# Performance work log

Measured on AMD Instinct MI355X. Metric: run time of the kernel, lower is better.

Reference implementation:

```python
import jax, jax.numpy as jnp
import numpy as np

N, D, R, E = 10000, 1024, 8, 80000


def setup_inputs() -> dict:
    key = jax.random.key(0)
    ks = jax.random.split(key, 8)
    s = 1.0 / np.sqrt(D)
    x = jax.random.normal(ks[0], (N, D), dtype=jnp.float32)
    edge_index = jax.random.randint(ks[1], (2, E), 0, N, dtype=jnp.int64)
    edge_type = jax.random.randint(ks[2], (E,), 0, R, dtype=jnp.int64)
    weight = jax.random.normal(ks[3], (R, D, D), dtype=jnp.float32) * s  # per-relation W_r
    root = jax.random.normal(ks[4], (D, D), dtype=jnp.float32) * s      # root/self-loop weight
    bias = jnp.zeros((D,), dtype=jnp.float32)
    w_gate = jax.random.normal(ks[5], (2 * D, D), dtype=jnp.float32) * (1.0 / np.sqrt(2 * D))
    b_gate = jnp.zeros((D,), dtype=jnp.float32)
    return {"x": x, "edge_index": edge_index, "edge_type": edge_type,
            "weight": weight, "root": root, "bias": bias,
            "w_gate": w_gate, "b_gate": b_gate}


def _rgcn(x, edge_index, edge_type, weight, root, bias):
    # PyG RGCNConv (aggr='mean'): per relation r, mean-aggregate x[src] into dst,
    # then transform by W_r (aggregate-then-transform, equivalent by linearity).
    src, dst = edge_index[0], edge_index[1]
    msgs = x[src]                                   # [E, D] gather
    out = x @ root + bias                           # root/self connection
    n = x.shape[0]
    for r in range(weight.shape[0]):                # small fixed relation loop
        mask = (edge_type == r).astype(x.dtype)     # [E]
        sums = jax.ops.segment_sum(msgs * mask[:, None], dst, num_segments=n)
        cnt = jax.ops.segment_sum(mask, dst, num_segments=n)
        mean = sums / jnp.maximum(cnt, 1.0)[:, None]
        out = out + mean @ weight[r]
    return out


def reference(x, edge_index, edge_type, weight, root, bias, w_gate, b_gate):
    u = _rgcn(x, edge_index, edge_type, weight, root, bias)
    # dropout p=0 -> identity
    z = jnp.concatenate([u, x], axis=1) @ w_gate + b_gate
    h = jnp.tanh(u) * z + x * (1.0 - z)
    return h
```

## Files before the change

kernel.cpp:

```cpp
#include <hip/hip_runtime.h>
#include <math.h>

typedef unsigned short u16;
typedef __attribute__((ext_vector_type(8))) short bf16x8;
typedef __attribute__((ext_vector_type(4))) float f32x4;

static constexpr int kN = 10000;
static constexpr int kNpad = 10240;
static constexpr int kD = 1024;
static constexpr int kR = 8;
static constexpr int kE = 80000;
static constexpr int kKz = 2 * kD;
static constexpr int kCrows = kNpad * (kR + 1);

#define GLB(p) ((const __attribute__((address_space(1))) unsigned int*)(const void*)(p))
#define LDSP(p) ((__attribute__((address_space(3))) unsigned int*)(p))

__device__ __forceinline__ u16 f2bf(float f) {
    union { float f; unsigned int i; } c; c.f = f;
    unsigned int u = c.i;
    return (u16)((u + 0x7FFFu + ((u >> 16) & 1u)) >> 16);
}
__device__ __forceinline__ float bf2f(u16 u) {
    union { unsigned int i; float f; } c; c.i = ((unsigned int)u) << 16;
    return c.f;
}
__device__ __forceinline__ ushort4 f2bf4(float4 v) {
    ushort4 o; o.x = f2bf(v.x); o.y = f2bf(v.y); o.z = f2bf(v.z); o.w = f2bf(v.w);
    return o;
}

__global__ void zero16(uint4* __restrict__ p, long n16) {
    long i = (long)blockIdx.x * blockDim.x + threadIdx.x;
    long st = (long)gridDim.x * blockDim.x;
    uint4 z = make_uint4(0, 0, 0, 0);
    for (; i < n16; i += st) p[i] = z;
}

__global__ void mark_edges(const int* __restrict__ src, const int* __restrict__ dst,
                           const int* __restrict__ etype,
                           int* __restrict__ cntd, int* __restrict__ flag) {
    int e = blockIdx.x * blockDim.x + threadIdx.x;
    if (e < kE) {
        atomicAdd(&cntd[dst[e]], 1);
        flag[etype[e] * kN + src[e]] = 1;
    }
}

__global__ __launch_bounds__(1024) void scan_combo(const int* __restrict__ cnt,
                                                   int* __restrict__ rowptr,
                                                   int* __restrict__ cursor,
                                                   const int* __restrict__ flag,
                                                   int* __restrict__ row_src,
                                                   int* __restrict__ pos_tab,
                                                   int* __restrict__ relcnt9) {
    __shared__ int wsum[16];
    __shared__ int carry;
    const int tid = threadIdx.x;
    const int lane = tid & 63;
    const int w = tid >> 6;

    if (blockIdx.x == 0) {
        if (tid == 0) carry = 0;
        const int nchunk = (kN + 1024) / 1024;
        for (int ch = 0; ch < nchunk; ++ch) {
            int idx = ch * 1024 + tid;
            int v = (idx < kN) ? cnt[idx] : 0;
            int s = v;
#pragma unroll
            for (int off = 1; off < 64; off <<= 1) {
                int t = __shfl_up(s, off, 64);
                if (lane >= off) s += t;
            }
            if (lane == 63) wsum[w] = s;
            __syncthreads();
            if (w == 0 && lane < 16) {
                int t = wsum[lane];
#pragma unroll
                for (int off = 1; off < 16; off <<= 1) {
                    int tt = __shfl_up(t, off, 64);
                    if (lane >= off) t += tt;
                }
                wsum[lane] = t;
            }
            __syncthreads();
            int wpre = (w > 0) ? wsum[w - 1] : 0;
            int incl = s + wpre + carry;
            int excl = incl - v;
            if (idx <= kN) rowptr[idx] = excl;
            if (idx < kN) cursor[idx] = 0;
            __syncthreads();
            if (tid == 1023) carry = incl;
            __syncthreads();
        }
        return;
    }

    const int rr = blockIdx.x - 1;
    if (rr == kR) {
        for (int i = tid; i < kNpad; i += 1024) row_src[i] = i;
        if (tid == 0) relcnt9[0] = kN;
        return;
    }
    const int r = rr;
    const int base = kNpad * (r + 1);
    if (tid == 0) carry = 0;
    const int nchunk = (kN + 1023) / 1024;
    for (int ch = 0; ch < nchunk; ++ch) {
        int idx = ch * 1024 + tid;
        int v = (idx < kN) ? flag[r * kN + idx] : 0;
        int s = v;
#pragma unroll
        for (int off = 1; off < 64; off <<= 1) {
            int t = __shfl_up(s, off, 64);
            if (lane >= off) s += t;
        }
        if (lane == 63) wsum[w] = s;
        __syncthreads();
        if (w == 0 && lane < 16) {
            int t = wsum[lane];
#pragma unroll
            for (int off = 1; off < 16; off <<= 1) {
                int tt = __shfl_up(t, off, 64);
                if (lane >= off) t += tt;
            }
            wsum[lane] = t;
        }
        __syncthreads();
        int wpre = (w > 0) ? wsum[w - 1] : 0;
        int incl = s + wpre + carry;
        int excl = incl - v;
        if (idx < kN && v) {
            row_src[base + excl] = idx;
            pos_tab[r * kN + idx] = base + excl;
        }
        __syncthreads();
        if (tid == 1023) carry = incl;
        __syncthreads();
    }
    if (tid == 0) relcnt9[r + 1] = carry;
}

__global__ void fill_edges(const int* __restrict__ src, const int* __restrict__ dst,
                           const int* __restrict__ etype, const int* __restrict__ rowptr,
                           int* __restrict__ cursor, const int* __restrict__ pos_tab,
                           int* __restrict__ erec) {
    int e = blockIdx.x * blockDim.x + threadIdx.x;
    if (e < kE) {
        int d = dst[e], r = etype[e], s = src[e];
        int pos = rowptr[d] + atomicAdd(&cursor[d], 1);
        erec[pos] = (pos_tab[r * kN + s] << 3) | r;
    }
}

__global__ void prep_ga(const float* __restrict__ x, u16* __restrict__ ga) {
    int row = blockIdx.x;
    int c = threadIdx.x << 2;
    if (row < kN) {
        float4 v = *reinterpret_cast<const float4*>(x + (size_t)row * kD + c);
        *reinterpret_cast<ushort4*>(ga + (size_t)row * kKz + kD + c) = f2bf4(v);
    } else {
        ushort4 z4;
        z4.x = 0; z4.y = 0; z4.z = 0; z4.w = 0;
        *reinterpret_cast<ushort4*>(ga + (size_t)row * kKz + c) = z4;
        *reinterpret_cast<ushort4*>(ga + (size_t)row * kKz + kD + c) = z4;
    }
}

__global__ void transpose_all(const float* __restrict__ root,
                              const float* __restrict__ weight,
                              const float* __restrict__ wgate,
                              u16* __restrict__ Bt9, u16* __restrict__ wg_t) {
    const int z = blockIdx.z;
    const float* S;
    u16* D;
    int ldD;
    if (z == 0)       { S = root;                              D = Bt9;                       ldD = kD; }
    else if (z <= 8)  { S = weight + (size_t)(z - 1) * kD * kD; D = Bt9 + (size_t)z * kD * kD; ldD = kD; }
    else              { S = wgate + (size_t)(z - 9) * kD * kD;  D = wg_t + (size_t)(z - 9) * kD; ldD = kKz; }
    __shared__ float t[32][33];
    int c0 = blockIdx.x * 32, r0 = blockIdx.y * 32;
    int x = threadIdx.x, y = threadIdx.y;
#pragma unroll
    for (int i = 0; i < 32; i += 8)
        t[y + i][x] = S[(size_t)(r0 + y + i) * kD + c0 + x];
    __syncthreads();
#pragma unroll
    for (int i = 0; i < 32; i += 8)
        D[(size_t)(c0 + y + i) * ldD + r0 + x] = f2bf(t[x][y + i]);
}

__global__ __launch_bounds__(256) void aggregate(const u16* __restrict__ yc,
                                                 const float* __restrict__ bias,
                                                 const int* __restrict__ rowptr,
                                                 const int* __restrict__ erec,
                                                 u16* __restrict__ ga) {
    const int d = blockIdx.x;
    const int c = threadIdx.x << 2;
    const int e0 = rowptr[d], e1 = rowptr[d + 1];

    __shared__ int cc8[kR];
    __shared__ float rs[kR];
    if (threadIdx.x < kR) cc8[threadIdx.x] = 0;
    __syncthreads();
    if (threadIdx.x < 64) {
        for (int e = e0 + threadIdx.x; e < e1; e += 64)
            atomicAdd(&cc8[erec[e] & 7], 1);
    }
    __syncthreads();
    if (threadIdx.x < kR)
        rs[threadIdx.x] = 1.0f / fmaxf((float)cc8[threadIdx.x], 1.0f);
    __syncthreads();

    ushort4 rv = *reinterpret_cast<const ushort4*>(yc + (size_t)d * kD + c);
    float4 bv = *reinterpret_cast<const float4*>(bias + c);
    float4 acc = make_float4(bf2f(rv.x) + bv.x, bf2f(rv.y) + bv.y,
                             bf2f(rv.z) + bv.z, bf2f(rv.w) + bv.w);

    int e = e0;
    for (; e + 3 < e1; e += 4) {
        int rec0 = erec[e], rec1 = erec[e + 1], rec2 = erec[e + 2], rec3 = erec[e + 3];
        ushort4 v0 = *reinterpret_cast<const ushort4*>(yc + (size_t)(rec0 >> 3) * kD + c);
        ushort4 v1 = *reinterpret_cast<const ushort4*>(yc + (size_t)(rec1 >> 3) * kD + c);
        ushort4 v2 = *reinterpret_cast<const ushort4*>(yc + (size_t)(rec2 >> 3) * kD + c);
        ushort4 v3 = *reinterpret_cast<const ushort4*>(yc + (size_t)(rec3 >> 3) * kD + c);
        float s0 = rs[rec0 & 7], s1 = rs[rec1 & 7], s2 = rs[rec2 & 7], s3 = rs[rec3 & 7];
        acc.x += s0 * bf2f(v0.x); acc.y += s0 * bf2f(v0.y);
        acc.z += s0 * bf2f(v0.z); acc.w += s0 * bf2f(v0.w);
        acc.x += s1 * bf2f(v1.x); acc.y += s1 * bf2f(v1.y);
        acc.z += s1 * bf2f(v1.z); acc.w += s1 * bf2f(v1.w);
        acc.x += s2 * bf2f(v2.x); acc.y += s2 * bf2f(v2.y);
        acc.z += s2 * bf2f(v2.z); acc.w += s2 * bf2f(v2.w);
        acc.x += s3 * bf2f(v3.x); acc.y += s3 * bf2f(v3.y);
        acc.z += s3 * bf2f(v3.z); acc.w += s3 * bf2f(v3.w);
    }
    for (; e < e1; ++e) {
        int rec = erec[e];
        float sc = rs[rec & 7];
        ushort4 v = *reinterpret_cast<const ushort4*>(yc + (size_t)(rec >> 3) * kD + c);
        acc.x += sc * bf2f(v.x); acc.y += sc * bf2f(v.y);
        acc.z += sc * bf2f(v.z); acc.w += sc * bf2f(v.w);
    }
    *reinterpret_cast<ushort4*>(ga + (size_t)d * kKz + c) = f2bf4(acc);
}

__global__ __launch_bounds__(512, 2) void gemm_compact(
    const u16* __restrict__ xb, int ldx,
    const u16* __restrict__ Bt9,
    const int* __restrict__ row_src, const int* __restrict__ relcnt9,
    u16* __restrict__ yc)
{
    const int t0 = blockIdx.y;
    const int relidx = t0 / 40;
    const int lt = t0 - relidx * 40;
    if (lt * 256 >= relcnt9[relidx]) return;

    __shared__ u16 sA[2][256 * 64];
    __shared__ u16 sB[2][256 * 64];

    const int tid = threadIdx.x;
    const int wave = tid >> 6;
    const int lane = tid & 63;

    const int row0 = t0 * 256;
    const int col0 = blockIdx.x * 256;

    const int s_row = tid >> 3;
    const int s_src = ((tid & 7) ^ (s_row & 7)) * 8;
    const int wbase = wave * 512;

    const u16* gA[4];
    const u16* gB[4];
#pragma unroll
    for (int q = 0; q < 4; ++q) {
        gA[q] = xb + (size_t)row_src[row0 + q * 64 + s_row] * ldx + s_src;
        gB[q] = Bt9 + (size_t)(relidx * kD + col0 + q * 64 + s_row) * kD + s_src;
    }

    auto stageA = [&](int b, int h) {
        u16* dA = &sA[b][0];
#pragma unroll
        for (int q = 2 * h; q < 2 * h + 2; ++q) {
            __builtin_amdgcn_global_load_lds(GLB(gA[q]), LDSP(dA + q * 4096 + wbase), 16, 0, 0);
            gA[q] += 64;
        }
    };
    auto stageB = [&](int b, int h) {
        u16* dB = &sB[b][0];
#pragma unroll
        for (int q = 2 * h; q < 2 * h + 2; ++q) {
            __builtin_amdgcn_global_load_lds(GLB(gB[q]), LDSP(dB + q * 4096 + wbase), 16, 0, 0);
            gB[q] += 64;
        }
    };

    const int wm = (wave >> 2) * 128;
    const int wn = (wave & 3) * 64;
    const int fm = lane & 15;
    const int g4 = lane >> 4;
    const int pc0 = ((g4) ^ (fm & 7)) * 8;
    const int pc1 = ((4 | g4) ^ (fm & 7)) * 8;

    f32x4 zf = {0.0f, 0.0f, 0.0f, 0.0f};
    f32x4 acc[8][4];
#pragma unroll
    for (int i = 0; i < 8; ++i)
#pragma unroll
        for (int j = 0; j < 4; ++j) acc[i][j] = zf;

    constexpr int T = kD / 64;
    stageA(0, 0); stageA(0, 1); stageB(0, 0); stageB(0, 1);
    stageB(1, 0); stageB(1, 1);

    bf16x8 af[8], bfl[4], bfh[4];

    for (int t = 0; t < T; ++t) {
        const int cb = t & 1, nb = cb ^ 1;
        const bool pf1 = (t + 1 < T);
        const bool pf2 = (t + 2 < T);
        const u16* cA = sA[cb];
        const u16* cB = sB[cb];

        if (pf1) stageA(nb, 0);
        if (t < T - 1) asm volatile("s_waitcnt vmcnt(6)" ::: "memory");
        else           asm volatile("s_waitcnt vmcnt(0)" ::: "memory");
        __builtin_amdgcn_s_barrier();
        asm volatile("" ::: "memory");
#pragma unroll
        for (int i = 0; i < 4; ++i) {
            af[2 * i]     = *reinterpret_cast<const bf16x8*>(&cA[(wm + i * 16 + fm) * 64 + pc0]);
            af[2 * i + 1] = *reinterpret_cast<const bf16x8*>(&cA[(wm + i * 16 + fm) * 64 + pc1]);
        }
#pragma unroll
        for (int j = 0; j < 2; ++j) {
            bfl[2 * j]     = *reinterpret_cast<const bf16x8*>(&cB[(wn + j * 16 + fm) * 64 + pc0]);
            bfl[2 * j + 1] = *reinterpret_cast<const bf16x8*>(&cB[(wn + j * 16 + fm) * 64 + pc1]);
        }
        __builtin_amdgcn_s_setprio(1);
#pragma unroll
        for (int i = 0; i < 4; ++i)
#pragma unroll
            for (int j = 0; j < 2; ++j) {
                acc[i][j] = __builtin_amdgcn_mfma_f32_16x16x32_bf16(bfl[2 * j], af[2 * i], acc[i][j], 0, 0, 0);
                acc[i][j] = __builtin_amdgcn_mfma_f32_16x16x32_bf16(bfl[2 * j + 1], af[2 * i + 1], acc[i][j], 0, 0, 0);
            }
        __builtin_amdgcn_s_setprio(0);

#pragma unroll
        for (int j = 0; j < 2; ++j) {
            bfh[2 * j]     = *reinterpret_cast<const bf16x8*>(&cB[(wn + 32 + j * 16 + fm) * 64 + pc0]);
            bfh[2 * j + 1] = *reinterpret_cast<const bf16x8*>(&cB[(wn + 32 + j * 16 + fm) * 64 + pc1]);
        }
        if (pf1) stageA(nb, 1);
        asm volatile("" ::: "memory");
        __builtin_amdgcn_s_barrier();
        asm volatile("" ::: "memory");
        __builtin_amdgcn_s_setprio(1);
#pragma unroll
        for (int i = 0; i < 4; ++i)
#pragma unroll
            for (int j = 0; j < 2; ++j) {
                acc[i][2 + j] = __builtin_amdgcn_mfma_f32_16x16x32_bf16(bfh[2 * j], af[2 * i], acc[i][2 + j], 0, 0, 0);
                acc[i][2 + j] = __builtin_amdgcn_mfma_f32_16x16x32_bf16(bfh[2 * j + 1], af[2 * i + 1], acc[i][2 + j], 0, 0, 0);
            }
        __builtin_amdgcn_s_setprio(0);

#pragma unroll
        for (int i = 0; i < 4; ++i) {
            af[2 * i]     = *reinterpret_cast<const bf16x8*>(&cA[(wm + 64 + i * 16 + fm) * 64 + pc0]);
            af[2 * i + 1] = *reinterpret_cast<const bf16x8*>(&cA[(wm + 64 + i * 16 + fm) * 64 + pc1]);
        }
        asm volatile("" ::: "memory");
        __builtin_amdgcn_s_barrier();
        asm volatile("" ::: "memory");
        __builtin_amdgcn_s_setprio(1);
#pragma unroll
        for (int i = 0; i < 4; ++i)
#pragma unroll
            for (int j = 0; j < 2; ++j) {
                acc[4 + i][2 + j] = __builtin_amdgcn_mfma_f32_16x16x32_bf16(bfh[2 * j], af[2 * i], acc[4 + i][2 + j], 0, 0, 0);
                acc[4 + i][2 + j] = __builtin_amdgcn_mfma_f32_16x16x32_bf16(bfh[2 * j + 1], af[2 * i + 1], acc[4 + i][2 + j], 0, 0, 0);
            }
        __builtin_amdgcn_s_setprio(0);

        if (pf2) { stageB(cb, 0); stageB(cb, 1); }
        asm volatile("" ::: "memory");
        __builtin_amdgcn_s_barrier();
        asm volatile("" ::: "memory");
        __builtin_amdgcn_s_setprio(1);
#pragma unroll
        for (int i = 0; i < 4; ++i)
#pragma unroll
            for (int j = 0; j < 2; ++j) {
                acc[4 + i][j] = __builtin_amdgcn_mfma_f32_16x16x32_bf16(bfl[2 * j], af[2 * i], acc[4 + i][j], 0, 0, 0);
                acc[4 + i][j] = __builtin_amdgcn_mfma_f32_16x16x32_bf16(bfl[2 * j + 1], af[2 * i + 1], acc[4 + i][j], 0, 0, 0);
            }
        __builtin_amdgcn_s_setprio(0);
    }

    const int cq = g4 * 4;
#pragma unroll
    for (int i = 0; i < 8; ++i) {
        int row = row0 + wm + i * 16 + fm;
#pragma unroll
        for (int j = 0; j < 4; ++j) {
            int col = col0 + wn + j * 16 + cq;
            f32x4 v = acc[i][j];
            ushort4 o;
            o.x = f2bf(v[0]); o.y = f2bf(v[1]); o.z = f2bf(v[2]); o.w = f2bf(v[3]);
            *reinterpret_cast<ushort4*>(yc + (size_t)row * kD + col) = o;
        }
    }
}

__global__ __launch_bounds__(256, 3) void gemm_mfma_gate(
    const u16* __restrict__ A, int lda,
    const u16* __restrict__ Bt, int ldb, int K,
    int M, const float* __restrict__ bias,
    float* __restrict__ Cf, const u16* __restrict__ uga, const float* __restrict__ xo)
{
    __shared__ u16 sA[3][128 * 32];
    __shared__ u16 sB[3][128 * 32];

    const int tid = threadIdx.x;
    const int wave = tid >> 6;
    const int lane = tid & 63;

    constexpr int GX = kD / 128;
    constexpr int GY = kNpad / 128;
    const int lin = blockIdx.y * GX + blockIdx.x;
    const int xcd = lin & 7;
    const int pos = lin >> 3;
    const int ty = xcd * (GY / 8) + (pos >> 3);
    const int tx = pos & 7;

    const int row0 = ty * 128;
    const int col0 = tx * 128;

    const int srow = wave * 16 + (lane >> 2);
    const int scol = (((lane & 3) ^ ((srow >> 1) & 3)) * 8);

    const u16* gA0 = A + (size_t)(row0 + srow) * lda + scol;
    const u16* gA1 = A + (size_t)(row0 + 64 + srow) * lda + scol;
    const u16* gB0 = Bt + (size_t)(col0 + srow) * ldb + scol;
    const u16* gB1 = Bt + (size_t)(col0 + 64 + srow) * ldb + scol;

    const int lof0 = (wave * 16) * 32;
    const int lof1 = (64 + wave * 16) * 32;

    const int mq = (wave >> 1) * 64;
    const int nq = (wave & 1) * 64;
    const int fm = lane & 15;
    const int fkx = (((lane >> 4) ^ ((fm >> 1) & 3))) * 8;

    f32x4 zf = {0.0f, 0.0f, 0.0f, 0.0f};
    f32x4 acc[4][4];
#pragma unroll
    for (int i = 0; i < 4; ++i)
#pragma unroll
        for (int j = 0; j < 4; ++j) acc[i][j] = zf;

    auto stage = [&](int s) {
        __builtin_amdgcn_global_load_lds(GLB(gA0), LDSP(sA[s] + lof0), 16, 0, 0);
        __builtin_amdgcn_global_load_lds(GLB(gA1), LDSP(sA[s] + lof1), 16, 0, 0);
        __builtin_amdgcn_global_load_lds(GLB(gB0), LDSP(sB[s] + lof0), 16, 0, 0);
        __builtin_amdgcn_global_load_lds(GLB(gB1), LDSP(sB[s] + lof1), 16, 0, 0);
        gA0 += 32; gA1 += 32; gB0 += 32; gB1 += 32;
    };

    const int T = K >> 5;
    stage(0);
    stage(1);

    int s = 0;
    for (int t = 0; t < T; ++t) {
        if (t + 2 < T) {
            stage(s == 0 ? 2 : (s - 1));
            asm volatile("s_waitcnt vmcnt(8)" ::: "memory");
        } else if (t + 1 < T) {
            asm volatile("s_waitcnt vmcnt(4)" ::: "memory");
        } else {
            asm volatile("s_waitcnt vmcnt(0)" ::: "memory");
        }
        __builtin_amdgcn_s_barrier();
        asm volatile("" ::: "memory");

        const u16* cA = sA[s];
        const u16* cB = sB[s];
        bf16x8 af[4], bfr[4];
#pragma unroll
        for (int i = 0; i < 4; ++i)
            af[i] = *reinterpret_cast<const bf16x8*>(&cA[(mq + i * 16 + fm) * 32 + fkx]);
#pragma unroll
        for (int j = 0; j < 4; ++j)
            bfr[j] = *reinterpret_cast<const bf16x8*>(&cB[(nq + j * 16 + fm) * 32 + fkx]);
#pragma unroll
        for (int i = 0; i < 4; ++i)
#pragma unroll
            for (int j = 0; j < 4; ++j)
                acc[i][j] = __builtin_amdgcn_mfma_f32_16x16x32_bf16(bfr[j], af[i], acc[i][j], 0, 0, 0);

        asm volatile("" ::: "memory");
        __builtin_amdgcn_s_barrier();
        s = (s == 2) ? 0 : (s + 1);
    }

    const int cq = (lane >> 4) * 4;
#pragma unroll
    for (int i = 0; i < 4; ++i) {
        int row = row0 + mq + i * 16 + fm;
        if (row >= M) continue;
#pragma unroll
        for (int j = 0; j < 4; ++j) {
            int col = col0 + nq + j * 16 + cq;
            f32x4 v = acc[i][j];
            float4 bv = *reinterpret_cast<const float4*>(bias + col);
            v[0] += bv.x; v[1] += bv.y; v[2] += bv.z; v[3] += bv.w;
            ushort4 ur = *reinterpret_cast<const ushort4*>(uga + (size_t)row * kKz + col);
            float4 xr = *reinterpret_cast<const float4*>(xo + (size_t)row * kD + col);
            float4 h;
            h.x = tanhf(bf2f(ur.x)) * v[0] + xr.x * (1.0f - v[0]);
            h.y = tanhf(bf2f(ur.y)) * v[1] + xr.y * (1.0f - v[1]);
            h.z = tanhf(bf2f(ur.z)) * v[2] + xr.z * (1.0f - v[2]);
            h.w = tanhf(bf2f(ur.w)) * v[3] + xr.w * (1.0f - v[3]);
            *reinterpret_cast<float4*>(Cf + (size_t)row * kD + col) = h;
        }
    }
}

extern "C" void kernel_launch(void* const* d_in, const int* in_sizes, int n_in,
                              void* d_out, int out_size, void* d_ws, size_t ws_size,
                              hipStream_t stream) {
    (void)in_sizes; (void)n_in; (void)out_size; (void)ws_size;

    const float* x     = (const float*)d_in[0];
    const int* eidx    = (const int*)d_in[1];
    const int* etype   = (const int*)d_in[2];
    const float* weight= (const float*)d_in[3];
    const float* root  = (const float*)d_in[4];
    const float* bias  = (const float*)d_in[5];
    const float* wgate = (const float*)d_in[6];
    const float* bgate = (const float*)d_in[7];
    float* out = (float*)d_out;

    const int* src = eidx;
    const int* dst = eidx + kE;

    char* ws = (char*)d_ws;
    size_t off = 0;
    u16* yc   = (u16*)(ws + off);    off += (size_t)kCrows * kD * 2;
    u16* ga   = (u16*)(ws + off);    off += (size_t)kNpad * kKz * 2;
    u16* Bt9  = (u16*)(ws + off);    off += (size_t)(kR + 1) * kD * kD * 2;
    u16* wg_t = (u16*)(ws + off);    off += (size_t)kD * kKz * 2;
    int* cntd    = (int*)(ws + off); off += (size_t)kN * 4;
    int* flag    = (int*)(ws + off); off += (size_t)kR * kN * 4;
    int* row_src = (int*)(ws + off); off += (size_t)kCrows * 4;
    int* pos_tab = (int*)(ws + off); off += (size_t)kR * kN * 4;
    int* rowp    = (int*)(ws + off); off += (size_t)(kN + 16) * 4;
    int* curs    = (int*)(ws + off); off += (size_t)kN * 4;
    int* erec    = (int*)(ws + off); off += (size_t)kE * 4;
    int* relcnt9 = (int*)(ws + off); off += 16 * 4;

    zero16<<<180, 256, 0, stream>>>((uint4*)cntd, (long)(kN + kR * kN + kCrows) / 4);

    mark_edges<<<(kE + 255) / 256, 256, 0, stream>>>(src, dst, etype, cntd, flag);

    scan_combo<<<kR + 2, 1024, 0, stream>>>(cntd, rowp, curs, flag, row_src,
                                            pos_tab, relcnt9);

    fill_edges<<<(kE + 255) / 256, 256, 0, stream>>>(src, dst, etype, rowp, curs,
                                                     pos_tab, erec);

    prep_ga<<<kNpad, 256, 0, stream>>>(x, ga);

    {
        dim3 b(32, 8);
        transpose_all<<<dim3(kD / 32, kD / 32, 11), b, 0, stream>>>(root, weight,
                                                                    wgate, Bt9, wg_t);
    }

    dim3 g1(kD / 256, kCrows / 256);
    gemm_compact<<<g1, 512, 0, stream>>>(ga + kD, kKz, Bt9, row_src, relcnt9, yc);

    aggregate<<<kN, 256, 0, stream>>>(yc, bias, rowp, erec, ga);

    dim3 g2(kD / 128, kNpad / 128);
    gemm_mfma_gate<<<g2, 256, 0, stream>>>(ga, kKz, wg_t, kKz, kKz, kN, bgate, out, ga, x);
}
```

Before: 443.2 us.

## Restructure gate GEMM main loop into K=64 double-buffered quadrant pipeline

The gate GEMM kernel moves from a three-stage K=32 LDS pipeline to a two-buffer K=64 scheme. A and B prefetches are split into halves and interleaved between four quadrant MFMA phases, with s_setprio raising priority around the MFMA bursts and a new XOR swizzle for 64-wide rows. The aim is to hide global-to-LDS latency and LDS reads behind matrix-core work, likely mirroring a schedule already used in the other GEMM. In exchange it adds more barriers per iteration and uses more LDS, so launch bounds drop to two blocks per CU.

```diff
diff --git a/kernel.cpp b/kernel.cpp
--- a/kernel.cpp
+++ b/kernel.cpp
@@ -413,14 +413,14 @@
     }
 }
 
-__global__ __launch_bounds__(256, 3) void gemm_mfma_gate(
+__global__ __launch_bounds__(256, 2) void gemm_mfma_gate(
     const u16* __restrict__ A, int lda,
     const u16* __restrict__ Bt, int ldb, int K,
     int M, const float* __restrict__ bias,
     float* __restrict__ Cf, const u16* __restrict__ uga, const float* __restrict__ xo)
 {
-    __shared__ u16 sA[3][128 * 32];
-    __shared__ u16 sB[3][128 * 32];
+    __shared__ u16 sA[2][128 * 64];
+    __shared__ u16 sB[2][128 * 64];
 
     const int tid = threadIdx.x;
     const int wave = tid >> 6;
@@ -437,21 +437,41 @@
     const int row0 = ty * 128;
     const int col0 = tx * 128;
 
-    const int srow = wave * 16 + (lane >> 2);
-    const int scol = (((lane & 3) ^ ((srow >> 1) & 3)) * 8);
-
-    const u16* gA0 = A + (size_t)(row0 + srow) * lda + scol;
-    const u16* gA1 = A + (size_t)(row0 + 64 + srow) * lda + scol;
-    const u16* gB0 = Bt + (size_t)(col0 + srow) * ldb + scol;
-    const u16* gB1 = Bt + (size_t)(col0 + 64 + srow) * ldb + scol;
-
-    const int lof0 = (wave * 16) * 32;
-    const int lof1 = (64 + wave * 16) * 32;
-
-    const int mq = (wave >> 1) * 64;
-    const int nq = (wave & 1) * 64;
+    const int s_row = tid >> 3;
+    const int s_src = ((tid & 7) ^ (s_row & 7)) * 8;
+    const int wbase = wave * 512;
+
+    const u16* gA[4];
+    const u16* gB[4];
+#pragma unroll
+    for (int q = 0; q < 4; ++q) {
+        gA[q] = A + (size_t)(row0 + q * 32 + s_row) * lda + s_src;
+        gB[q] = Bt + (size_t)(col0 + q * 32 + s_row) * ldb + s_src;
+    }
+
+    auto stageA = [&](int b, int h) {
+        u16* dA = &sA[b][0];
+#pragma unroll
+        for (int q = 2 * h; q < 2 * h + 2; ++q) {
+            __builtin_amdgcn_global_load_lds(GLB(gA[q]), LDSP(dA + q * 2048 + wbase), 16, 0, 0);
+            gA[q] += 64;
+        }
+    };
+    auto stageB = [&](int b, int h) {
+        u16* dB = &sB[b][0];
+#pragma unroll
+        for (int q = 2 * h; q < 2 * h + 2; ++q) {
+            __builtin_amdgcn_global_load_lds(GLB(gB[q]), LDSP(dB + q * 2048 + wbase), 16, 0, 0);
+            gB[q] += 64;
+        }
+    };
+
+    const int wm = (wave >> 1) * 64;
+    const int wn = (wave & 1) * 64;
     const int fm = lane & 15;
-    const int fkx = (((lane >> 4) ^ ((fm >> 1) & 3))) * 8;
+    const int g4 = lane >> 4;
+    const int pc0 = ((g4) ^ (fm & 7)) * 8;
+    const int pc1 = ((4 | g4) ^ (fm & 7)) * 8;
 
     f32x4 zf = {0.0f, 0.0f, 0.0f, 0.0f};
     f32x4 acc[4][4];
@@ -460,59 +480,104 @@
 #pragma unroll
         for (int j = 0; j < 4; ++j) acc[i][j] = zf;
 
-    auto stage = [&](int s) {
-        __builtin_amdgcn_global_load_lds(GLB(gA0), LDSP(sA[s] + lof0), 16, 0, 0);
-        __builtin_amdgcn_global_load_lds(GLB(gA1), LDSP(sA[s] + lof1), 16, 0, 0);
-        __builtin_amdgcn_global_load_lds(GLB(gB0), LDSP(sB[s] + lof0), 16, 0, 0);
-        __builtin_amdgcn_global_load_lds(GLB(gB1), LDSP(sB[s] + lof1), 16, 0, 0);
-        gA0 += 32; gA1 += 32; gB0 += 32; gB1 += 32;
-    };
-
-    const int T = K >> 5;
-    stage(0);
-    stage(1);
-
-    int s = 0;
+    const int T = K >> 6;
+    stageA(0, 0); stageA(0, 1); stageB(0, 0); stageB(0, 1);
+    stageB(1, 0); stageB(1, 1);
+
+    bf16x8 af[4], bfl[4], bfh[4];
+
     for (int t = 0; t < T; ++t) {
-        if (t + 2 < T) {
-            stage(s == 0 ? 2 : (s - 1));
-            asm volatile("s_waitcnt vmcnt(8)" ::: "memory");
-        } else if (t + 1 < T) {
-            asm volatile("s_waitcnt vmcnt(4)" ::: "memory");
-        } else {
-            asm volatile("s_waitcnt vmcnt(0)" ::: "memory");
-        }
-        __builtin_amdgcn_s_barrier();
-        asm volatile("" ::: "memory");
-
-        const u16* cA = sA[s];
-        const u16* cB = sB[s];
-        bf16x8 af[4], bfr[4];
-#pragma unroll
-        for (int i = 0; i < 4; ++i)
-            af[i] = *reinterpret_cast<const bf16x8*>(&cA[(mq + i * 16 + fm) * 32 + fkx]);
-#pragma unroll
-        for (int j = 0; j < 4; ++j)
-            bfr[j] = *reinterpret_cast<const bf16x8*>(&cB[(nq + j * 16 + fm) * 32 + fkx]);
-#pragma unroll
-        for (int i = 0; i < 4; ++i)
-#pragma unroll
-            for (int j = 0; j < 4; ++j)
-                acc[i][j] = __builtin_amdgcn_mfma_f32_16x16x32_bf16(bfr[j], af[i], acc[i][j], 0, 0, 0);
-
-        asm volatile("" ::: "memory");
-        __builtin_amdgcn_s_barrier();
-        s = (s == 2) ? 0 : (s + 1);
-    }
-
-    const int cq = (lane >> 4) * 4;
+        const int cb = t & 1, nb = cb ^ 1;
+        const bool pf1 = (t + 1 < T);
+        const bool pf2 = (t + 2 < T);
+        const u16* cA = sA[cb];
+        const u16* cB = sB[cb];
+
+        if (pf1) stageA(nb, 0);
+        if (t < T - 1) asm volatile("s_waitcnt vmcnt(6)" ::: "memory");
+        else           asm volatile("s_waitcnt vmcnt(0)" ::: "memory");
+        __builtin_amdgcn_s_barrier();
+        asm volatile("" ::: "memory");
+#pragma unroll
+        for (int i = 0; i < 2; ++i) {
+            af[2 * i]     = *reinterpret_cast<const bf16x8*>(&cA[(wm + i * 16 + fm) * 64 + pc0]);
+            af[2 * i + 1] = *reinterpret_cast<const bf16x8*>(&cA[(wm + i * 16 + fm) * 64 + pc1]);
+        }
+#pragma unroll
+        for (int j = 0; j < 2; ++j) {
+            bfl[2 * j]     = *reinterpret_cast<const bf16x8*>(&cB[(wn + j * 16 + fm) * 64 + pc0]);
+            bfl[2 * j + 1] = *reinterpret_cast<const bf16x8*>(&cB[(wn + j * 16 + fm) * 64 + pc1]);
+        }
+        __builtin_amdgcn_s_setprio(1);
+#pragma unroll
+        for (int i = 0; i < 2; ++i)
+#pragma unroll
+            for (int j = 0; j < 2; ++j) {
+                acc[i][j] = __builtin_amdgcn_mfma_f32_16x16x32_bf16(bfl[2 * j], af[2 * i], acc[i][j], 0, 0, 0);
+                acc[i][j] = __builtin_amdgcn_mfma_f32_16x16x32_bf16(bfl[2 * j + 1], af[2 * i + 1], acc[i][j], 0, 0, 0);
+            }
+        __builtin_amdgcn_s_setprio(0);
+
+#pragma unroll
+        for (int j = 0; j < 2; ++j) {
+            bfh[2 * j]     = *reinterpret_cast<const bf16x8*>(&cB[(wn + 32 + j * 16 + fm) * 64 + pc0]);
+            bfh[2 * j + 1] = *reinterpret_cast<const bf16x8*>(&cB[(wn + 32 + j * 16 + fm) * 64 + pc1]);
+        }
+        if (pf1) stageA(nb, 1);
+        asm volatile("" ::: "memory");
+        __builtin_amdgcn_s_barrier();
+        asm volatile("" ::: "memory");
+        __builtin_amdgcn_s_setprio(1);
+#pragma unroll
+        for (int i = 0; i < 2; ++i)
+#pragma unroll
+            for (int j = 0; j < 2; ++j) {
+                acc[i][2 + j] = __builtin_amdgcn_mfma_f32_16x16x32_bf16(bfh[2 * j], af[2 * i], acc[i][2 + j], 0, 0, 0);
+                acc[i][2 + j] = __builtin_amdgcn_mfma_f32_16x16x32_bf16(bfh[2 * j + 1], af[2 * i + 1], acc[i][2 + j], 0, 0, 0);
+            }
+        __builtin_amdgcn_s_setprio(0);
+
+#pragma unroll
+        for (int i = 0; i < 2; ++i) {
+            af[2 * i]     = *reinterpret_cast<const bf16x8*>(&cA[(wm + 32 + i * 16 + fm) * 64 + pc0]);
+            af[2 * i + 1] = *reinterpret_cast<const bf16x8*>(&cA[(wm + 32 + i * 16 + fm) * 64 + pc1]);
+        }
+        asm volatile("" ::: "memory");
+        __builtin_amdgcn_s_barrier();
+        asm volatile("" ::: "memory");
+        __builtin_amdgcn_s_setprio(1);
+#pragma unroll
+        for (int i = 0; i < 2; ++i)
+#pragma unroll
+            for (int j = 0; j < 2; ++j) {
+                acc[2 + i][2 + j] = __builtin_amdgcn_mfma_f32_16x16x32_bf16(bfh[2 * j], af[2 * i], acc[2 + i][2 + j], 0, 0, 0);
+                acc[2 + i][2 + j] = __builtin_amdgcn_mfma_f32_16x16x32_bf16(bfh[2 * j + 1], af[2 * i + 1], acc[2 + i][2 + j], 0, 0, 0);
+            }
+        __builtin_amdgcn_s_setprio(0);
+
+        if (pf2) { stageB(cb, 0); stageB(cb, 1); }
+        asm volatile("" ::: "memory");
+        __builtin_amdgcn_s_barrier();
+        asm volatile("" ::: "memory");
+        __builtin_amdgcn_s_setprio(1);
+#pragma unroll
+        for (int i = 0; i < 2; ++i)
+#pragma unroll
+            for (int j = 0; j < 2; ++j) {
+                acc[2 + i][j] = __builtin_amdgcn_mfma_f32_16x16x32_bf16(bfl[2 * j], af[2 * i], acc[2 + i][j], 0, 0, 0);
+                acc[2 + i][j] = __builtin_amdgcn_mfma_f32_16x16x32_bf16(bfl[2 * j + 1], af[2 * i + 1], acc[2 + i][j], 0, 0, 0);
+            }
+        __builtin_amdgcn_s_setprio(0);
+    }
+
+    const int cq = g4 * 4;
 #pragma unroll
     for (int i = 0; i < 4; ++i) {
-        int row = row0 + mq + i * 16 + fm;
+        int row = row0 + wm + i * 16 + fm;
         if (row >= M) continue;
 #pragma unroll
         for (int j = 0; j < 4; ++j) {
-            int col = col0 + nq + j * 16 + cq;
+            int col = col0 + wn + j * 16 + cq;
             f32x4 v = acc[i][j];
             float4 bv = *reinterpret_cast<const float4*>(bias + col);
             v[0] += bv.x; v[1] += bv.y; v[2] += bv.z; v[3] += bv.w;
```

Result: slower. 481.2 us (+8.6%).
